# Kernel tuning notes

Hardware: AMD Instinct MI355X
Metric: run time of the kernel (lower is better)

Reference implementation:

```python
import jax, jax.numpy as jnp
import numpy as np

N, T, D, H = 64, 512, 512, 512

def setup_inputs() -> dict:
    key = jax.random.key(0)
    k1, k2, k3, k4 = jax.random.split(key, 4)
    x = jax.random.normal(k1, (N, T, D), dtype=jnp.float32)
    h0 = jax.random.normal(k2, (N, H), dtype=jnp.float32)
    Wx = jax.random.normal(k3, (D, H), dtype=jnp.float32) / jnp.sqrt(jnp.float32(D))
    Wh = jax.random.normal(k4, (H, H), dtype=jnp.float32) / jnp.sqrt(jnp.float32(H))
    b = jnp.zeros((H,), dtype=jnp.float32)
    return {"x": x, "h0": h0, "Wx": Wx, "Wh": Wh, "b": b}

def reference(x, h0, Wx, Wh, b):
    # Precompute the input projection for all timesteps as one big GEMM:
    # (N, T, D) @ (D, H) -> (N, T, H)
    xw = jnp.einsum('ntd,dh->nth', x, Wx) + b
    xw_t = jnp.swapaxes(xw, 0, 1)  # (T, N, H) for scan over time

    def step(prev_h, xw_step):
        next_h = jnp.tanh(prev_h @ Wh + xw_step)
        return next_h, next_h

    _, hs = jax.lax.scan(step, h0, xw_t)  # hs: (T, N, H)
    return jnp.swapaxes(hs, 0, 1)  # (N, T, H)
```

## Files before the change

### kernel.cpp

```cpp
#include <hip/hip_runtime.h>


typedef __attribute__((ext_vector_type(8))) short short8;
typedef __attribute__((ext_vector_type(4))) float f32x4;

#define DIM 512
#define T_S 512

union Frag { uint4 v; short8 s; unsigned short u[8]; };

static __device__ __forceinline__ unsigned short f2bf(float f) {
  union { float f; unsigned u; } v;
  v.f = f;
  unsigned r = v.u + 0x7FFFu + ((v.u >> 16) & 1u);
  return (unsigned short)(r >> 16);
}

static __device__ __forceinline__ unsigned cvt_pk_bf16(float a, float b) {
  unsigned r;
  asm("v_cvt_pk_bf16_f32 %0, %1, %2" : "=v"(r) : "v"(a), "v"(b));
  return r;
}

static __device__ __forceinline__ float fast_tanh(float s) {
  float e = __builtin_amdgcn_exp2f(2.885390082f * s);
  return 1.0f - 2.0f * __builtin_amdgcn_rcpf(e + 1.0f);
}

__global__ __launch_bounds__(64) void prepack(const float* __restrict__ Wx,
                                              const float* __restrict__ Wh,
                                              uint4* __restrict__ wxb,
                                              uint4* __restrict__ whb) {
  int bid = blockIdx.x;
  int mat = bid >> 9;
  int idx = bid & 511;
  int kk = idx >> 5, cc = idx & 31;
  int lane = threadIdx.x;
  int lo = lane & 15, hi = lane >> 4;
  const float* src = mat ? Wh : Wx;
  uint4* dst = mat ? whb : wxb;
  int col = cc * 16 + lo;
  int kbase = kk * 32 + hi * 8;
  Frag fr;
#pragma unroll
  for (int j = 0; j < 8; ++j)
    fr.u[j] = f2bf(src[(size_t)(kbase + j) * DIM + col]);
  dst[(kk * 32 + cc) * 64 + lane] = fr.v;
}

__global__ __launch_bounds__(256) void gemm_xw(const float* __restrict__ x,
                                               const uint4* __restrict__ wxb,
                                               const float* __restrict__ bias,
                                               float* __restrict__ out) {
  int bid = blockIdx.x;
  int m = bid >> 2, nb = bid & 3;
  int wave = threadIdx.x >> 6, lane = threadIdx.x & 63;
  int lo = lane & 15, hi = lane >> 4;
  int rowbase = m * 64;
  int colbase = nb * 128 + wave * 32;

  f32x4 acc[4][2];
#pragma unroll
  for (int mi = 0; mi < 4; ++mi)
#pragma unroll
    for (int ni = 0; ni < 2; ++ni) acc[mi][ni] = (f32x4){0.f, 0.f, 0.f, 0.f};

  for (int kk = 0; kk < 16; ++kk) {
    short8 afrag[4];
#pragma unroll
    for (int mi = 0; mi < 4; ++mi) {
      const float* ap = x + (size_t)(rowbase + mi * 16 + lo) * DIM + kk * 32 + hi * 8;
      float4 f0 = *(const float4*)ap;
      float4 f1 = *(const float4*)(ap + 4);
      Frag a;
      a.u[0] = f2bf(f0.x); a.u[1] = f2bf(f0.y); a.u[2] = f2bf(f0.z); a.u[3] = f2bf(f0.w);
      a.u[4] = f2bf(f1.x); a.u[5] = f2bf(f1.y); a.u[6] = f2bf(f1.z); a.u[7] = f2bf(f1.w);
      afrag[mi] = a.s;
    }
#pragma unroll
    for (int ni = 0; ni < 2; ++ni) {
      int cc = nb * 8 + wave * 2 + ni;
      Frag b;
      b.v = wxb[(kk * 32 + cc) * 64 + lane];
#pragma unroll
      for (int mi = 0; mi < 4; ++mi)
        acc[mi][ni] = __builtin_amdgcn_mfma_f32_16x16x32_bf16(afrag[mi], b.s, acc[mi][ni], 0, 0, 0);
    }
  }
#pragma unroll
  for (int ni = 0; ni < 2; ++ni) {
    int col = colbase + ni * 16 + lo;
    float bv = bias[col];
#pragma unroll
    for (int mi = 0; mi < 4; ++mi)
#pragma unroll
      for (int r = 0; r < 4; ++r) {
        int row = rowbase + mi * 16 + hi * 4 + r;
        out[(size_t)row * DIM + col] = acc[mi][ni][r] + bv;
      }
  }
}

__shared__ uint4 wlds[4][32][64];
__shared__ unsigned short hbuf2[2][16 * 512];

template <int BUF>
static __device__ __forceinline__ void step_body(
    int t, int w, int lane, const uint4 (&bw)[12][4],
    const uint4* const (&rdp)[8], uint2* const (&wrp)[4],
    float (&xwv)[16], float*& gp) {
  f32x4 acc[4];
#pragma unroll
  for (int i = 0; i < 4; ++i)
    acc[i] = (f32x4){xwv[i * 4 + 0], xwv[i * 4 + 1], xwv[i * 4 + 2], xwv[i * 4 + 3]};

  const float* lp = gp + ((t < T_S - 1) ? DIM : 0);
#pragma unroll
  for (int i = 0; i < 4; ++i) {
    float4 f = *(const float4*)(lp + i * 16);
    xwv[i * 4 + 0] = f.x; xwv[i * 4 + 1] = f.y;
    xwv[i * 4 + 2] = f.z; xwv[i * 4 + 3] = f.w;
  }

#pragma unroll
  for (int kk = 0; kk < 12; ++kk) {
    Frag hf; hf.v = rdp[kk & 7][((kk & 8) ? 32 : 0) + BUF * 1024];
#pragma unroll
    for (int i = 0; i < 4; ++i) {
      Frag a; a.v = bw[kk][i];
      acc[i] = __builtin_amdgcn_mfma_f32_16x16x32_bf16(a.s, hf.s, acc[i], 0, 0, 0);
    }
  }
#pragma unroll
  for (int kk = 12; kk < 16; ++kk) {
    Frag hf; hf.v = rdp[kk & 7][32 + BUF * 1024];
#pragma unroll
    for (int i = 0; i < 4; ++i) {
      Frag a; a.v = wlds[kk - 12][w * 4 + i][lane];
      acc[i] = __builtin_amdgcn_mfma_f32_16x16x32_bf16(a.s, hf.s, acc[i], 0, 0, 0);
    }
  }

#pragma unroll
  for (int i = 0; i < 4; ++i) {
    float h0 = fast_tanh(acc[i][0]);
    float h1 = fast_tanh(acc[i][1]);
    float h2 = fast_tanh(acc[i][2]);
    float h3 = fast_tanh(acc[i][3]);
    *(float4*)(gp + i * 16) = (float4){h0, h1, h2, h3};
    uint2 u;
    u.x = cvt_pk_bf16(h0, h1);
    u.y = cvt_pk_bf16(h2, h3);
    wrp[i][(BUF ^ 1) * 2048] = u;
  }
  gp += DIM;

  asm volatile("s_waitcnt lgkmcnt(0)" ::: "memory");
  __builtin_amdgcn_sched_barrier(0);
  __builtin_amdgcn_s_barrier();
  __builtin_amdgcn_sched_barrier(0);
}

__global__ __launch_bounds__(512, 2) void rnn_scan(const float* __restrict__ h0,
                                                   const uint4* __restrict__ whb,
                                                   float* __restrict__ out) {
  int g = blockIdx.x;
  int w = threadIdx.x >> 6, lane = threadIdx.x & 63;
  int lo = lane & 15, hi = lane >> 4;
  int msk = (lo & 7) << 4;

  uint4 bw[12][4];
#pragma unroll
  for (int kk = 0; kk < 12; ++kk)
#pragma unroll
    for (int i = 0; i < 4; ++i)
      bw[kk][i] = whb[(kk * 32 + (w * 4 + i)) * 64 + lane];

#pragma unroll
  for (int e = 0; e < 16; ++e) {
    int idx = e * 512 + threadIdx.x;
    int s = idx >> 11, rem = idx & 2047;
    wlds[s][rem >> 6][rem & 63] = whb[((12 + s) * 32 + (rem >> 6)) * 64 + (rem & 63)];
  }

  const uint4* rdp[8];
#pragma unroll
  for (int kk = 0; kk < 8; ++kk)
    rdp[kk] = (const uint4*)((const char*)hbuf2 + lo * 1024 + ((kk * 64 + hi * 16) ^ msk));
  uint2* wrp[4];
#pragma unroll
  for (int i = 0; i < 4; ++i)
    wrp[i] = (uint2*)((char*)hbuf2 + lo * 1024 + ((128 * w + 32 * i + 8 * hi) ^ msk));

#pragma unroll
  for (int i = 0; i < 4; ++i) {
    const float* hp = h0 + (size_t)(g * 16 + lo) * DIM + w * 64 + i * 16 + hi * 4;
    float4 f = *(const float4*)hp;
    uint2 u;
    u.x = (unsigned)f2bf(f.x) | ((unsigned)f2bf(f.y) << 16);
    u.y = (unsigned)f2bf(f.z) | ((unsigned)f2bf(f.w) << 16);
    wrp[i][0] = u;
  }

  float* gp = out + ((size_t)(g * 16 + lo) * T_S) * DIM + w * 64 + hi * 4;

  float xwv[16];
#pragma unroll
  for (int i = 0; i < 4; ++i) {
    float4 f = *(const float4*)(gp + i * 16);
    xwv[i * 4 + 0] = f.x; xwv[i * 4 + 1] = f.y;
    xwv[i * 4 + 2] = f.z; xwv[i * 4 + 3] = f.w;
  }

  __syncthreads();

#pragma unroll 1
  for (int t = 0; t < T_S; t += 2) {
    step_body<0>(t,     w, lane, bw, rdp, wrp, xwv, gp);
    step_body<1>(t + 1, w, lane, bw, rdp, wrp, xwv, gp);
  }
}

extern "C" void kernel_launch(void* const* d_in, const int* in_sizes, int n_in,
                              void* d_out, int out_size, void* d_ws, size_t ws_size,
                              hipStream_t stream) {
  const float* x  = (const float*)d_in[0];
  const float* h0 = (const float*)d_in[1];
  const float* Wx = (const float*)d_in[2];
  const float* Wh = (const float*)d_in[3];
  const float* b  = (const float*)d_in[4];
  float* out = (float*)d_out;

  char* ws = (char*)d_ws;
  uint4* whb = (uint4*)ws;
  uint4* wxb = (uint4*)(ws + 524288);

  prepack<<<1024, 64, 0, stream>>>(Wx, Wh, wxb, whb);
  gemm_xw<<<2048, 256, 0, stream>>>(x, wxb, b, out);
  rnn_scan<<<4, 512, 0, stream>>>(h0, whb, out);
}
```

Measured before the change: 1.201 ms.

## Split Wh residency across registers, LDS, and per-step global/L2 streaming

Reduces register-resident Wh slices from 12 to 8 K-chunks, keeps 4 chunks in LDS, and streams the last 4 chunks from global memory (L2-cached) every timestep, prefetched ahead of the MFMA loops. This frees VGPRs, which may relieve register pressure or spilling, at the cost of extra global loads on the serial recurrence critical path each step.

After: 2.297 ms. +91.3%, slower.

```diff
diff --git a/kernel.cpp b/kernel.cpp
--- a/kernel.cpp
+++ b/kernel.cpp
@@ -106,7 +106,8 @@
 
 template <int BUF>
 static __device__ __forceinline__ void step_body(
-    int t, int w, int lane, const uint4 (&bw)[12][4],
+    int t, int w, int lane, const uint4 (&bw)[8][4],
+    const uint4* const (&wp)[4],
     const uint4* const (&rdp)[8], uint2* const (&wrp)[4],
     float (&xwv)[16], float*& gp) {
   f32x4 acc[4];
@@ -122,21 +123,44 @@
     xwv[i * 4 + 2] = f.z; xwv[i * 4 + 3] = f.w;
   }
 
-#pragma unroll
-  for (int kk = 0; kk < 12; ++kk) {
-    Frag hf; hf.v = rdp[kk & 7][((kk & 8) ? 32 : 0) + BUF * 1024];
+  uint4 swA[2][4];
+#pragma unroll
+  for (int k2 = 0; k2 < 2; ++k2)
+#pragma unroll
+    for (int i = 0; i < 4; ++i) swA[k2][i] = wp[k2][i * 64];
+
+#pragma unroll
+  for (int kk = 0; kk < 8; ++kk) {
+    Frag hf; hf.v = rdp[kk][BUF * 1024];
 #pragma unroll
     for (int i = 0; i < 4; ++i) {
       Frag a; a.v = bw[kk][i];
       acc[i] = __builtin_amdgcn_mfma_f32_16x16x32_bf16(a.s, hf.s, acc[i], 0, 0, 0);
     }
   }
+
+  uint4 swB[2][4];
+#pragma unroll
+  for (int k2 = 0; k2 < 2; ++k2)
+#pragma unroll
+    for (int i = 0; i < 4; ++i) swB[k2][i] = wp[2 + k2][i * 64];
+
+#pragma unroll
+  for (int kk = 8; kk < 12; ++kk) {
+    Frag hf; hf.v = rdp[kk & 7][32 + BUF * 1024];
+#pragma unroll
+    for (int i = 0; i < 4; ++i) {
+      Frag a; a.v = wlds[kk - 8][w * 4 + i][lane];
+      acc[i] = __builtin_amdgcn_mfma_f32_16x16x32_bf16(a.s, hf.s, acc[i], 0, 0, 0);
+    }
+  }
+
 #pragma unroll
   for (int kk = 12; kk < 16; ++kk) {
     Frag hf; hf.v = rdp[kk & 7][32 + BUF * 1024];
 #pragma unroll
     for (int i = 0; i < 4; ++i) {
-      Frag a; a.v = wlds[kk - 12][w * 4 + i][lane];
+      Frag a; a.v = (kk < 14) ? swA[kk - 12][i] : swB[kk - 14][i];
       acc[i] = __builtin_amdgcn_mfma_f32_16x16x32_bf16(a.s, hf.s, acc[i], 0, 0, 0);
     }
   }
@@ -169,9 +193,9 @@
   int lo = lane & 15, hi = lane >> 4;
   int msk = (lo & 7) << 4;
 
-  uint4 bw[12][4];
-#pragma unroll
-  for (int kk = 0; kk < 12; ++kk)
+  uint4 bw[8][4];
+#pragma unroll
+  for (int kk = 0; kk < 8; ++kk)
 #pragma unroll
     for (int i = 0; i < 4; ++i)
       bw[kk][i] = whb[(kk * 32 + (w * 4 + i)) * 64 + lane];
@@ -180,8 +204,13 @@
   for (int e = 0; e < 16; ++e) {
     int idx = e * 512 + threadIdx.x;
     int s = idx >> 11, rem = idx & 2047;
-    wlds[s][rem >> 6][rem & 63] = whb[((12 + s) * 32 + (rem >> 6)) * 64 + (rem & 63)];
-  }
+    wlds[s][rem >> 6][rem & 63] = whb[((8 + s) * 32 + (rem >> 6)) * 64 + (rem & 63)];
+  }
+
+  const uint4* wp[4];
+#pragma unroll
+  for (int k = 0; k < 4; ++k)
+    wp[k] = whb + ((12 + k) * 32 + w * 4) * 64 + lane;
 
   const uint4* rdp[8];
 #pragma unroll
@@ -216,8 +245,8 @@
 
 #pragma unroll 1
   for (int t = 0; t < T_S; t += 2) {
-    step_body<0>(t,     w, lane, bw, rdp, wrp, xwv, gp);
-    step_body<1>(t + 1, w, lane, bw, rdp, wrp, xwv, gp);
+    step_body<0>(t,     w, lane, bw, wp, rdp, wrp, xwv, gp);
+    step_body<1>(t + 1, w, lane, bw, wp, rdp, wrp, xwv, gp);
   }
 }
 
```
